# Kernel optimization log

Measured on AMD Instinct MI355X. Metric: run time of the kernel, lower is better.

Reference implementation:

```python
import jax, jax.numpy as jnp
import numpy as np

HEAD_NUM = 16
ROPE_BASE = 10000.0


def _rotate_half(x):
    # interleaved pairs: (x0,x1,x2,x3,...) -> (-x1,x0,-x3,x2,...)
    x_even = x[..., ::2]
    x_odd = x[..., 1::2]
    return jnp.stack((-x_odd, x_even), axis=-1).reshape(x.shape)


def _rope_cos_sin(seq_len, head_dim):
    half = head_dim // 2
    inv_freq = 1.0 / (ROPE_BASE ** (jnp.arange(half, dtype=jnp.float32) / half))
    t = jnp.arange(seq_len, dtype=jnp.float32)
    freqs = t[:, None] * inv_freq[None, :]            # [S, half]
    cos = jnp.repeat(jnp.cos(freqs), 2, axis=-1)       # [S, D]
    sin = jnp.repeat(jnp.sin(freqs), 2, axis=-1)       # [S, D]
    return cos, sin


def setup_inputs() -> dict:
    key = jax.random.key(0)
    ks = jax.random.split(key, 9)
    B, S, H = 2, 2048, 2048
    std = 1.0 / np.sqrt(H)
    return {
        "x": jax.random.normal(ks[0], (B, S, H), jnp.float32),
        "Wq": jax.random.normal(ks[1], (H, H), jnp.float32) * std,
        "bq": jax.random.normal(ks[2], (H,), jnp.float32) * std,
        "Wk": jax.random.normal(ks[3], (H, H), jnp.float32) * std,
        "bk": jax.random.normal(ks[4], (H,), jnp.float32) * std,
        "Wv": jax.random.normal(ks[5], (H, H), jnp.float32) * std,
        "bv": jax.random.normal(ks[6], (H,), jnp.float32) * std,
        "Wo": jax.random.normal(ks[7], (H, H), jnp.float32) * std,
        "bo": jax.random.normal(ks[8], (H,), jnp.float32) * std,
    }


def reference(x, Wq, bq, Wk, bk, Wv, bv, Wo, bo):
    B, S, H = x.shape
    nh = HEAD_NUM
    d = H // nh
    scale = jnp.float32(np.sqrt(d))

    def proj(W, b):
        y = x @ W.T + b                                 # torch Linear: x W^T + b
        return y.reshape(B, S, nh, d).transpose(0, 2, 1, 3)  # [B, nh, S, d]

    Q = proj(Wq, bq)
    K = proj(Wk, bk)
    V = proj(Wv, bv)

    cos, sin = _rope_cos_sin(S, d)                      # [S, d]
    Q = Q * cos + _rotate_half(Q) * sin
    K = K * cos + _rotate_half(K) * sin

    scores = jnp.einsum("bhqd,bhkd->bhqk", Q, K) / scale  # [B, nh, S, S]
    causal = jnp.tril(jnp.ones((S, S), dtype=bool))
    scores = jnp.where(causal, scores, jnp.float32(-jnp.inf))
    attn = jax.nn.softmax(scores, axis=-1)
    out = jnp.einsum("bhqk,bhkd->bhqd", attn, V)        # [B, nh, S, d]
    out = out.transpose(0, 2, 1, 3).reshape(B, S, H)
    return out @ Wo.T + bo
```

## Files before the change

### kernel.cpp

```cpp
#include <hip/hip_runtime.h>
#include <math.h>

typedef __bf16 bf16x8 __attribute__((ext_vector_type(8)));
typedef float floatx4 __attribute__((ext_vector_type(4)));

__device__ __forceinline__ unsigned short f32_to_bf16(float f) {
  unsigned int u = __float_as_uint(f);
  u = u + 0x7FFFu + ((u >> 16) & 1u);
  return (unsigned short)(u >> 16);
}
__device__ __forceinline__ float bf16_to_f32(unsigned short s) {
  return __uint_as_float(((unsigned int)s) << 16);
}

__device__ __forceinline__ void gld_lds16(const unsigned short* g,
                                          unsigned short* l) {
  __builtin_amdgcn_global_load_lds(
      (const __attribute__((address_space(1))) unsigned int*)g,
      (__attribute__((address_space(3))) unsigned int*)l, 16, 0, 0);
}

__global__ void cast_kernel(const float* __restrict__ in,
                            unsigned short* __restrict__ out, int n4) {
  int i = blockIdx.x * blockDim.x + threadIdx.x;
  if (i >= n4) return;
  const float4 v = reinterpret_cast<const float4*>(in)[i];
  ushort4 o;
  o.x = f32_to_bf16(v.x); o.y = f32_to_bf16(v.y);
  o.z = f32_to_bf16(v.z); o.w = f32_to_bf16(v.w);
  reinterpret_cast<ushort4*>(out)[i] = o;
}

__global__ void cast4_kernel(const float* __restrict__ a,
                             const float* __restrict__ b,
                             const float* __restrict__ c,
                             const float* __restrict__ d,
                             unsigned short* __restrict__ oa,
                             unsigned short* __restrict__ ob,
                             unsigned short* __restrict__ oc,
                             unsigned short* __restrict__ od, int n4) {
  int i = blockIdx.x * blockDim.x + threadIdx.x;
  if (i >= n4) return;
  const float* in;
  unsigned short* out;
  switch (blockIdx.y) {
    case 0: in = a; out = oa; break;
    case 1: in = b; out = ob; break;
    case 2: in = c; out = oc; break;
    default: in = d; out = od; break;
  }
  const float4 v = reinterpret_cast<const float4*>(in)[i];
  ushort4 o;
  o.x = f32_to_bf16(v.x); o.y = f32_to_bf16(v.y);
  o.z = f32_to_bf16(v.z); o.w = f32_to_bf16(v.w);
  reinterpret_cast<ushort4*>(out)[i] = o;
}

__global__ void rope_table_kernel(float2* __restrict__ tab, int total) {
  int idx = blockIdx.x * blockDim.x + threadIdx.x;
  if (idx >= total) return;
  const int s = idx >> 6, i = idx & 63;
  const float inv = powf(10000.0f, -(float)i * (1.0f / 64.0f));
  const float ang = (float)s * inv;
  tab[idx] = make_float2(cosf(ang), sinf(ang));
}

template <int EPI>
__global__ __launch_bounds__(256) void gemm_fused(
    const unsigned short* __restrict__ A, const unsigned short* __restrict__ B,
    const float* __restrict__ bias, float* __restrict__ Cf,
    unsigned short* __restrict__ Cb, const float2* __restrict__ tab,
    float scl, int M, int N, int K, int S) {
  __shared__ unsigned short As[128 * 64];
  __shared__ unsigned short Bs[128 * 64];
  const int t = threadIdx.x;
  const int lane = t & 63;
  const int w = t >> 6;

  const int nwg = gridDim.x * gridDim.y;
  const int orig = blockIdx.y * gridDim.x + blockIdx.x;
  const int wgid = (orig & 7) * (nwg >> 3) + (orig >> 3);
  const int bm = (wgid / gridDim.x) * 128;
  const int bn = (wgid % gridDim.x) * 128;

  const int wm = (w & 1) * 64;
  const int wn = (w >> 1) * 64;
  const int m16 = lane & 15;
  const int quad = lane >> 4;
  const int key = m16 & 7;

  const int lr = lane >> 3;
  const int lc = ((lane & 7) ^ lr) * 8;

  floatx4 acc[4][4];
#pragma unroll
  for (int i = 0; i < 4; ++i)
#pragma unroll
    for (int j = 0; j < 4; ++j) acc[i][j] = floatx4{0.f, 0.f, 0.f, 0.f};

  const unsigned short* Abase = A + (size_t)(bm + w * 32 + lr) * K + lc;
  const unsigned short* Bbase = B + (size_t)(bn + w * 32 + lr) * K + lc;

  for (int k0 = 0; k0 < K; k0 += 64) {
    __syncthreads();
#pragma unroll
    for (int it = 0; it < 4; ++it) {
      gld_lds16(Abase + (size_t)it * 8 * K + k0, &As[(w * 4 + it) * 512]);
      gld_lds16(Bbase + (size_t)it * 8 * K + k0, &Bs[(w * 4 + it) * 512]);
    }
    __syncthreads();
#pragma unroll
    for (int ks = 0; ks < 64; ks += 32) {
      const int ck = ks >> 3;
      bf16x8 af[4], bfr[4];
#pragma unroll
      for (int i = 0; i < 4; ++i)
        af[i] = *reinterpret_cast<const bf16x8*>(
            &As[(wm + i * 16 + m16) * 64 + ((ck | quad) ^ key) * 8]);
#pragma unroll
      for (int j = 0; j < 4; ++j)
        bfr[j] = *reinterpret_cast<const bf16x8*>(
            &Bs[(wn + j * 16 + m16) * 64 + ((ck | quad) ^ key) * 8]);
#pragma unroll
      for (int i = 0; i < 4; ++i)
#pragma unroll
        for (int j = 0; j < 4; ++j)
          acc[i][j] = __builtin_amdgcn_mfma_f32_16x16x32_bf16(
              af[i], bfr[j], acc[i][j], 0, 0, 0);
    }
  }

#pragma unroll
  for (int i = 0; i < 4; ++i) {
    const int rbase = bm + wm + i * 16 + quad * 4;
#pragma unroll
    for (int j = 0; j < 4; ++j) {
      const int col = bn + wn + j * 16 + m16;
      const float bv = bias[col];
      if (EPI == 0) {
#pragma unroll
        for (int r = 0; r < 4; ++r)
          Cf[(size_t)(rbase + r) * N + col] = acc[i][j][r] + bv;
      } else if (EPI == 1) {
        const int pi = (col & 127) >> 1;
#pragma unroll
        for (int r = 0; r < 4; ++r) {
          const int row = rbase + r;
          const int s = row & (S - 1);
          const float v = acc[i][j][r] + bv;
          const float vp = __shfl_xor(v, 1);
          const float2 cs = tab[s * 64 + pi];
          const float oe = (v * cs.x - vp * cs.y) * scl;
          const float oo = (vp * cs.x + v * cs.y) * scl;
          if ((m16 & 1) == 0) {
            const unsigned pk =
                (unsigned)f32_to_bf16(oe) | ((unsigned)f32_to_bf16(oo) << 16);
            *reinterpret_cast<unsigned*>(Cb + (size_t)row * N + col) = pk;
          }
        }
      } else {
        const int b = rbase >> 11;
        const int s = rbase & (S - 1);
        ushort4 pk;
        pk.x = f32_to_bf16(acc[i][j][0] + bv);
        pk.y = f32_to_bf16(acc[i][j][1] + bv);
        pk.z = f32_to_bf16(acc[i][j][2] + bv);
        pk.w = f32_to_bf16(acc[i][j][3] + bv);
        *reinterpret_cast<ushort4*>(
            Cb + ((size_t)((b << 11) + col)) * S + s) = pk;
      }
    }
  }
}

constexpr int F_BQ = 128, F_BK = 64, F_DH = 128;
constexpr int KS_STR = 136;
constexpr int VS_STR = 72;
constexpr int PS_STR = 72;

__global__ __launch_bounds__(256, 2) void fattn_kernel(
    const unsigned short* __restrict__ Qb, const unsigned short* __restrict__ Kb,
    const unsigned short* __restrict__ Vtb, unsigned short* __restrict__ Ob,
    int S, int H, int nh) {
  __shared__ unsigned short Ks[F_BK * KS_STR];
  __shared__ unsigned short Vts[F_DH * VS_STR];
  __shared__ unsigned short Ps[F_BQ * PS_STR];

  const int t = threadIdx.x;
  const int lane = t & 63;
  const int w = t >> 6;
  const int l15 = lane & 15;
  const int quad = lane >> 4;

  const int i = blockIdx.x;
  const int bh = i & 31;
  const int qt = (i < 256) ? (i >> 5) : (15 - ((i - 256) >> 5));
  const int h = bh & 15;
  const int b = bh >> 4;
  const int q0 = qt * F_BQ;

  const unsigned short* Qrow = Qb + ((size_t)(b * S + q0)) * H + h * F_DH;
  const unsigned short* Krow = Kb + ((size_t)b * S) * H + h * F_DH;
  const unsigned short* Vtrow = Vtb + ((size_t)bh * F_DH) * S;
  unsigned short* Orow = Ob + ((size_t)(b * S + q0)) * H + h * F_DH;

  bf16x8 aq[2][4];
#pragma unroll
  for (int qg = 0; qg < 2; ++qg)
#pragma unroll
    for (int ks = 0; ks < 4; ++ks)
      aq[qg][ks] = *reinterpret_cast<const bf16x8*>(
          Qrow + (size_t)(w * 32 + qg * 16 + l15) * H + ks * 32 + quad * 8);

  floatx4 oacc[2][8];
#pragma unroll
  for (int qg = 0; qg < 2; ++qg)
#pragma unroll
    for (int dj = 0; dj < 8; ++dj) oacc[qg][dj] = floatx4{0.f, 0.f, 0.f, 0.f};
  float lpart[2][4] = {{0.f, 0.f, 0.f, 0.f}, {0.f, 0.f, 0.f, 0.f}};
  int qrow[2][4];
#pragma unroll
  for (int qg = 0; qg < 2; ++qg)
#pragma unroll
    for (int r = 0; r < 4; ++r)
      qrow[qg][r] = q0 + w * 32 + qg * 16 + quad * 4 + r;

  const int ntile = q0 / F_BK + 2;
  for (int tile = 0; tile < ntile; ++tile) {
    const int k0 = tile * F_BK;
    __syncthreads();
    {
      const int kt = t >> 2, c0 = (t & 3) * 32;
      const unsigned short* g = Krow + (size_t)(k0 + kt) * H + c0;
#pragma unroll
      for (int ii = 0; ii < 4; ++ii)
        *reinterpret_cast<uint4*>(&Ks[kt * KS_STR + c0 + ii * 8]) =
            *reinterpret_cast<const uint4*>(g + ii * 8);
    }
    {
      const int d = t >> 1, c0 = (t & 1) * 32;
      const unsigned short* g = Vtrow + (size_t)d * S + k0 + c0;
#pragma unroll
      for (int ii = 0; ii < 4; ++ii)
        *reinterpret_cast<uint4*>(&Vts[d * VS_STR + c0 + ii * 8]) =
            *reinterpret_cast<const uint4*>(g + ii * 8);
    }
    __syncthreads();

    floatx4 sacc[2][4];
#pragma unroll
    for (int qg = 0; qg < 2; ++qg)
#pragma unroll
      for (int j = 0; j < 4; ++j) sacc[qg][j] = floatx4{0.f, 0.f, 0.f, 0.f};
#pragma unroll
    for (int j = 0; j < 4; ++j) {
      bf16x8 bk[4];
#pragma unroll
      for (int ks = 0; ks < 4; ++ks)
        bk[ks] = *reinterpret_cast<const bf16x8*>(
            &Ks[(j * 16 + l15) * KS_STR + ks * 32 + quad * 8]);
#pragma unroll
      for (int qg = 0; qg < 2; ++qg)
#pragma unroll
        for (int ks = 0; ks < 4; ++ks)
          sacc[qg][j] = __builtin_amdgcn_mfma_f32_16x16x32_bf16(
              aq[qg][ks], bk[ks], sacc[qg][j], 0, 0, 0);
    }

#pragma unroll
    for (int qg = 0; qg < 2; ++qg)
#pragma unroll
      for (int j = 0; j < 4; ++j) {
        const int ktg = k0 + j * 16 + l15;
#pragma unroll
        for (int r = 0; r < 4; ++r) {
          const float p =
              (ktg <= qrow[qg][r]) ? exp2f(sacc[qg][j][r]) : 0.0f;
          lpart[qg][r] += p;
          Ps[(w * 32 + qg * 16 + quad * 4 + r) * PS_STR + j * 16 + l15] =
              f32_to_bf16(p);
        }
      }

#pragma unroll
    for (int ks2 = 0; ks2 < 2; ++ks2) {
      bf16x8 ap[2];
#pragma unroll
      for (int qg = 0; qg < 2; ++qg)
        ap[qg] = *reinterpret_cast<const bf16x8*>(
            &Ps[(w * 32 + qg * 16 + l15) * PS_STR + ks2 * 32 + quad * 8]);
#pragma unroll
      for (int dj = 0; dj < 8; ++dj) {
        const bf16x8 bv = *reinterpret_cast<const bf16x8*>(
            &Vts[(dj * 16 + l15) * VS_STR + ks2 * 32 + quad * 8]);
#pragma unroll
        for (int qg = 0; qg < 2; ++qg)
          oacc[qg][dj] = __builtin_amdgcn_mfma_f32_16x16x32_bf16(
              ap[qg], bv, oacc[qg][dj], 0, 0, 0);
      }
    }
  }

#pragma unroll
  for (int qg = 0; qg < 2; ++qg)
#pragma unroll
    for (int r = 0; r < 4; ++r) {
      float l = lpart[qg][r];
      l += __shfl_xor(l, 1);
      l += __shfl_xor(l, 2);
      l += __shfl_xor(l, 4);
      l += __shfl_xor(l, 8);
      const float linv = 1.0f / l;
      unsigned short* orow =
          Orow + (size_t)(w * 32 + qg * 16 + quad * 4 + r) * H;
#pragma unroll
      for (int dj = 0; dj < 8; ++dj)
        orow[dj * 16 + l15] = f32_to_bf16(oacc[qg][dj][r] * linv);
    }
}

extern "C" void kernel_launch(void* const* d_in, const int* in_sizes, int n_in,
                              void* d_out, int out_size, void* d_ws,
                              size_t ws_size, hipStream_t stream) {
  const float* x  = (const float*)d_in[0];
  const float* Wq = (const float*)d_in[1];
  const float* bq = (const float*)d_in[2];
  const float* Wk = (const float*)d_in[3];
  const float* bk = (const float*)d_in[4];
  const float* Wv = (const float*)d_in[5];
  const float* bv = (const float*)d_in[6];
  const float* Wo = (const float*)d_in[7];
  const float* bo = (const float*)d_in[8];
  float* out = (float*)d_out;

  const int B = 2, S = 2048, H = 2048, nh = 16;
  const int M = B * S;

  unsigned short* Wqb = (unsigned short*)d_ws;
  unsigned short* Wkb = Wqb + (size_t)H * H;
  unsigned short* Wvb = Wkb + (size_t)H * H;
  unsigned short* Wob = Wvb + (size_t)H * H;
  unsigned short* xb  = Wob + (size_t)H * H;
  unsigned short* Qbb = xb + (size_t)M * H;
  unsigned short* Kbb = Qbb + (size_t)M * H;
  unsigned short* Vtb = Kbb + (size_t)M * H;
  unsigned short* Ob  = Vtb + (size_t)M * H;
  float2* tab = (float2*)(Ob + (size_t)M * H);

  const int cast_w4 = H * H / 4;
  const int cast_x4 = M * H / 4;
  const int tab_n = S * 64;

  rope_table_kernel<<<dim3(tab_n / 256), dim3(256), 0, stream>>>(tab, tab_n);
  cast_kernel<<<dim3(cast_x4 / 256), dim3(256), 0, stream>>>(x, xb, cast_x4);
  cast4_kernel<<<dim3(cast_w4 / 256, 4), dim3(256), 0, stream>>>(
      Wq, Wk, Wv, Wo, Wqb, Wkb, Wvb, Wob, cast_w4);

  dim3 ggrid(H / 128, M / 128);
  const float qscale = 0.08838834764831845f * 1.4426950408889634f;

  gemm_fused<1><<<ggrid, dim3(256), 0, stream>>>(
      xb, Wqb, bq, nullptr, Qbb, tab, qscale, M, H, H, S);
  gemm_fused<1><<<ggrid, dim3(256), 0, stream>>>(
      xb, Wkb, bk, nullptr, Kbb, tab, 1.0f, M, H, H, S);
  gemm_fused<2><<<ggrid, dim3(256), 0, stream>>>(
      xb, Wvb, bv, nullptr, Vtb, nullptr, 1.0f, M, H, H, S);

  fattn_kernel<<<dim3((S / F_BQ) * B * nh), dim3(256), 0, stream>>>(
      Qbb, Kbb, Vtb, Ob, S, H, nh);

  gemm_fused<0><<<ggrid, dim3(256), 0, stream>>>(
      Ob, Wob, bo, out, nullptr, nullptr, 1.0f, M, H, H, S);
}
```

Baseline: 435.5 us.

## Use 256x256 double-buffered GEMM tiles and fuse QKV projections into one launch

Replaces the 128x128 single-buffered GEMM with a 512-thread 256x256 tile kernel. Its LDS is double-buffered: the next K-slice is prefetched with global_load_lds while MFMAs run on the current one, and s_setprio raises priority around the MFMA blocks. The Q, K and V projections become one launch, with blockIdx.z choosing weights, bias, output and epilogue. The goal is more operand reuse, overlap of loads with compute, and fewer launches. The cost is fewer workgroups: 384 for QKV and only 128 for the output projection on a 256-CU part, which risks idle CUs and wave-quantization tails.

```diff
diff --git a/kernel.cpp b/kernel.cpp
--- a/kernel.cpp
+++ b/kernel.cpp
@@ -65,89 +65,130 @@
   tab[idx] = make_float2(cosf(ang), sinf(ang));
 }
 
-template <int EPI>
-__global__ __launch_bounds__(256) void gemm_fused(
-    const unsigned short* __restrict__ A, const unsigned short* __restrict__ B,
-    const float* __restrict__ bias, float* __restrict__ Cf,
-    unsigned short* __restrict__ Cb, const float2* __restrict__ tab,
-    float scl, int M, int N, int K, int S) {
-  __shared__ unsigned short As[128 * 64];
-  __shared__ unsigned short Bs[128 * 64];
+template <int MODE>
+__global__ __launch_bounds__(512, 1) void gemm256(
+    const unsigned short* __restrict__ A,
+    const unsigned short* __restrict__ B0,
+    const unsigned short* __restrict__ B1,
+    const unsigned short* __restrict__ B2,
+    const float* __restrict__ bias0, const float* __restrict__ bias1,
+    const float* __restrict__ bias2, float* __restrict__ Cf,
+    unsigned short* __restrict__ Cb0, unsigned short* __restrict__ Cb1,
+    unsigned short* __restrict__ Cb2, const float2* __restrict__ tab,
+    float qscale, int M, int N, int K, int S) {
+  __shared__ unsigned short As[2][256 * 64];
+  __shared__ unsigned short Bs[2][256 * 64];
   const int t = threadIdx.x;
   const int lane = t & 63;
   const int w = t >> 6;
+  const int wmh = w >> 2;
+  const int wnq = w & 3;
+  const int m16 = lane & 15;
+  const int quad = lane >> 4;
+  const int key = m16 & 7;
+  const int z = (MODE == 1) ? blockIdx.z : 0;
 
   const int nwg = gridDim.x * gridDim.y;
   const int orig = blockIdx.y * gridDim.x + blockIdx.x;
   const int wgid = (orig & 7) * (nwg >> 3) + (orig >> 3);
-  const int bm = (wgid / gridDim.x) * 128;
-  const int bn = (wgid % gridDim.x) * 128;
-
-  const int wm = (w & 1) * 64;
-  const int wn = (w >> 1) * 64;
-  const int m16 = lane & 15;
-  const int quad = lane >> 4;
-  const int key = m16 & 7;
+  const int bm = (wgid / gridDim.x) * 256;
+  const int bn = (wgid % gridDim.x) * 256;
+
+  const unsigned short* B =
+      (MODE == 0) ? B0 : ((z == 0) ? B0 : ((z == 1) ? B1 : B2));
+  const float* bias =
+      (MODE == 0) ? bias0 : ((z == 0) ? bias0 : ((z == 1) ? bias1 : bias2));
+  unsigned short* Cb =
+      (MODE == 0) ? (unsigned short*)0 : ((z == 0) ? Cb0 : ((z == 1) ? Cb1 : Cb2));
+  const float scl = (z == 0) ? qscale : 1.0f;
 
   const int lr = lane >> 3;
   const int lc = ((lane & 7) ^ lr) * 8;
-
-  floatx4 acc[4][4];
-#pragma unroll
-  for (int i = 0; i < 4; ++i)
-#pragma unroll
-    for (int j = 0; j < 4; ++j) acc[i][j] = floatx4{0.f, 0.f, 0.f, 0.f};
-
-  const unsigned short* Abase = A + (size_t)(bm + w * 32 + lr) * K + lc;
-  const unsigned short* Bbase = B + (size_t)(bn + w * 32 + lr) * K + lc;
-
-  for (int k0 = 0; k0 < K; k0 += 64) {
+  const unsigned short* Ag = A + (size_t)(bm + w * 32 + lr) * K + lc;
+  const unsigned short* Bg = B + (size_t)(bn + w * 32 + lr) * K + lc;
+
+  floatx4 acc[8][4];
+#pragma unroll
+  for (int mi = 0; mi < 8; ++mi)
+#pragma unroll
+    for (int ni = 0; ni < 4; ++ni) acc[mi][ni] = floatx4{0.f, 0.f, 0.f, 0.f};
+
+#pragma unroll
+  for (int it = 0; it < 4; ++it) {
+    gld_lds16(Ag + (size_t)it * 8 * K, &As[0][(w * 4 + it) * 512]);
+    gld_lds16(Bg + (size_t)it * 8 * K, &Bs[0][(w * 4 + it) * 512]);
+  }
+
+  const int nkt = K >> 6;
+  for (int kt = 0; kt < nkt; ++kt) {
+    const int cur = kt & 1;
     __syncthreads();
-#pragma unroll
-    for (int it = 0; it < 4; ++it) {
-      gld_lds16(Abase + (size_t)it * 8 * K + k0, &As[(w * 4 + it) * 512]);
-      gld_lds16(Bbase + (size_t)it * 8 * K + k0, &Bs[(w * 4 + it) * 512]);
-    }
-    __syncthreads();
-#pragma unroll
-    for (int ks = 0; ks < 64; ks += 32) {
-      const int ck = ks >> 3;
-      bf16x8 af[4], bfr[4];
-#pragma unroll
-      for (int i = 0; i < 4; ++i)
-        af[i] = *reinterpret_cast<const bf16x8*>(
-            &As[(wm + i * 16 + m16) * 64 + ((ck | quad) ^ key) * 8]);
-#pragma unroll
-      for (int j = 0; j < 4; ++j)
-        bfr[j] = *reinterpret_cast<const bf16x8*>(
-            &Bs[(wn + j * 16 + m16) * 64 + ((ck | quad) ^ key) * 8]);
-#pragma unroll
-      for (int i = 0; i < 4; ++i)
-#pragma unroll
-        for (int j = 0; j < 4; ++j)
-          acc[i][j] = __builtin_amdgcn_mfma_f32_16x16x32_bf16(
-              af[i], bfr[j], acc[i][j], 0, 0, 0);
+    const unsigned short* Ac = &As[cur][0];
+    const unsigned short* Bc = &Bs[cur][0];
+    unsigned short* An = &As[cur ^ 1][0];
+    unsigned short* Bn = &Bs[cur ^ 1][0];
+    const bool pf = (kt + 1 < nkt);
+    const int kn = (kt + 1) << 6;
+
+#pragma unroll
+    for (int q = 0; q < 4; ++q) {
+      const int mh = q >> 1, nh = q & 1;
+      bf16x8 af[4][2], bfr[2][2];
+#pragma unroll
+      for (int mi = 0; mi < 4; ++mi) {
+        const int mrow = wmh * 128 + (mh * 4 + mi) * 16 + m16;
+#pragma unroll
+        for (int ks = 0; ks < 2; ++ks)
+          af[mi][ks] = *reinterpret_cast<const bf16x8*>(
+              &Ac[mrow * 64 + (((ks * 4 + quad) ^ key) << 3)]);
+      }
+#pragma unroll
+      for (int ni = 0; ni < 2; ++ni) {
+        const int nrow = wnq * 64 + (nh * 2 + ni) * 16 + m16;
+#pragma unroll
+        for (int ks = 0; ks < 2; ++ks)
+          bfr[ni][ks] = *reinterpret_cast<const bf16x8*>(
+              &Bc[nrow * 64 + (((ks * 4 + quad) ^ key) << 3)]);
+      }
+      if (pf) {
+        gld_lds16(Ag + (size_t)q * 8 * K + kn, &An[(w * 4 + q) * 512]);
+        gld_lds16(Bg + (size_t)q * 8 * K + kn, &Bn[(w * 4 + q) * 512]);
+      }
+      __builtin_amdgcn_s_barrier();
+      __builtin_amdgcn_s_setprio(1);
+#pragma unroll
+      for (int mi = 0; mi < 4; ++mi)
+#pragma unroll
+        for (int ni = 0; ni < 2; ++ni)
+#pragma unroll
+          for (int ks = 0; ks < 2; ++ks)
+            acc[mh * 4 + mi][nh * 2 + ni] =
+                __builtin_amdgcn_mfma_f32_16x16x32_bf16(
+                    af[mi][ks], bfr[ni][ks], acc[mh * 4 + mi][nh * 2 + ni],
+                    0, 0, 0);
+      __builtin_amdgcn_s_setprio(0);
+      __builtin_amdgcn_s_barrier();
     }
   }
 
 #pragma unroll
-  for (int i = 0; i < 4; ++i) {
-    const int rbase = bm + wm + i * 16 + quad * 4;
-#pragma unroll
-    for (int j = 0; j < 4; ++j) {
-      const int col = bn + wn + j * 16 + m16;
-      const float bv = bias[col];
-      if (EPI == 0) {
+  for (int mi = 0; mi < 8; ++mi) {
+    const int rbase = bm + wmh * 128 + mi * 16 + quad * 4;
+#pragma unroll
+    for (int ni = 0; ni < 4; ++ni) {
+      const int col = bn + wnq * 64 + ni * 16 + m16;
+      const float bvv = bias[col];
+      if (MODE == 0) {
 #pragma unroll
         for (int r = 0; r < 4; ++r)
-          Cf[(size_t)(rbase + r) * N + col] = acc[i][j][r] + bv;
-      } else if (EPI == 1) {
+          Cf[(size_t)(rbase + r) * N + col] = acc[mi][ni][r] + bvv;
+      } else if (z != 2) {
         const int pi = (col & 127) >> 1;
 #pragma unroll
         for (int r = 0; r < 4; ++r) {
           const int row = rbase + r;
           const int s = row & (S - 1);
-          const float v = acc[i][j][r] + bv;
+          const float v = acc[mi][ni][r] + bvv;
           const float vp = __shfl_xor(v, 1);
           const float2 cs = tab[s * 64 + pi];
           const float oe = (v * cs.x - vp * cs.y) * scl;
@@ -162,10 +203,10 @@
         const int b = rbase >> 11;
         const int s = rbase & (S - 1);
         ushort4 pk;
-        pk.x = f32_to_bf16(acc[i][j][0] + bv);
-        pk.y = f32_to_bf16(acc[i][j][1] + bv);
-        pk.z = f32_to_bf16(acc[i][j][2] + bv);
-        pk.w = f32_to_bf16(acc[i][j][3] + bv);
+        pk.x = f32_to_bf16(acc[mi][ni][0] + bvv);
+        pk.y = f32_to_bf16(acc[mi][ni][1] + bvv);
+        pk.z = f32_to_bf16(acc[mi][ni][2] + bvv);
+        pk.w = f32_to_bf16(acc[mi][ni][3] + bvv);
         *reinterpret_cast<ushort4*>(
             Cb + ((size_t)((b << 11) + col)) * S + s) = pk;
       }
@@ -356,19 +397,16 @@
   cast4_kernel<<<dim3(cast_w4 / 256, 4), dim3(256), 0, stream>>>(
       Wq, Wk, Wv, Wo, Wqb, Wkb, Wvb, Wob, cast_w4);
 
-  dim3 ggrid(H / 128, M / 128);
   const float qscale = 0.08838834764831845f * 1.4426950408889634f;
 
-  gemm_fused<1><<<ggrid, dim3(256), 0, stream>>>(
-      xb, Wqb, bq, nullptr, Qbb, tab, qscale, M, H, H, S);
-  gemm_fused<1><<<ggrid, dim3(256), 0, stream>>>(
-      xb, Wkb, bk, nullptr, Kbb, tab, 1.0f, M, H, H, S);
-  gemm_fused<2><<<ggrid, dim3(256), 0, stream>>>(
-      xb, Wvb, bv, nullptr, Vtb, nullptr, 1.0f, M, H, H, S);
+  gemm256<1><<<dim3(H / 256, M / 256, 3), dim3(512), 0, stream>>>(
+      xb, Wqb, Wkb, Wvb, bq, bk, bv, nullptr, Qbb, Kbb, Vtb, tab, qscale,
+      M, H, H, S);
 
   fattn_kernel<<<dim3((S / F_BQ) * B * nh), dim3(256), 0, stream>>>(
       Qbb, Kbb, Vtb, Ob, S, H, nh);
 
-  gemm_fused<0><<<ggrid, dim3(256), 0, stream>>>(
-      Ob, Wob, bo, out, nullptr, nullptr, 1.0f, M, H, H, S);
-}
+  gemm256<0><<<dim3(H / 256, M / 256, 1), dim3(512), 0, stream>>>(
+      Ob, Wob, nullptr, nullptr, bo, nullptr, nullptr, out, nullptr, nullptr,
+      nullptr, nullptr, 1.0f, M, H, H, S);
+}
```

New measurement: 468.9 us. +7.7%, slower.
